# Kernel optimization log

Measured on AMD Instinct MI355X. Metric: run time of the kernel, lower is better.

## Reference

```python
import jax, jax.numpy as jnp
import numpy as np

T = 10
EPS = 1e-05

def setup_inputs() -> dict:
    key = jax.random.key(0)
    k1, k2 = jax.random.split(key)
    B, C, H, W = 128, 64, 56, 56
    X = jax.random.normal(k1, (B, C, H, W), dtype=jnp.float32)
    beta = jnp.zeros((C,), dtype=jnp.float32)
    return {"X": X, "beta": beta}


def reference(X, beta):
    # Training-path of BWItnBlock.forward (grad enabled branch of iter_norm_batch)
    B, C, H, W = X.shape
    d = C                      # n_channels, num_groups g = 1
    m = B * H * W
    # x = X.transpose(0,1).view(g, d, -1)  -> [d, m] with g=1
    x = jnp.transpose(X, (1, 0, 2, 3)).reshape(d, m)
    mean = jnp.mean(x, axis=1, keepdims=True)          # [d, 1]
    xc = x - mean                                      # [d, m]
    I = jnp.eye(d, dtype=X.dtype)
    # Sigma = eps*I + xc xc^T / m
    Sigma = EPS * I + (xc @ xc.T) / m                  # [d, d]
    # fix_cov: multiply off-diagonal by 0.9, diagonal by 1.0
    fix = 0.9 + 0.1 * I
    Sigma = Sigma * fix
    rTr = 1.0 / jnp.trace(Sigma)                       # scalar (sum(Sigma * I))
    Sigma_N = Sigma * rTr
    # Newton-Schulz iterations for inverse sqrt: P <- 1.5 P - 0.5 P^3 Sigma_N
    P = I
    for _ in range(T):
        P = 1.5 * P - 0.5 * ((P @ P @ P) @ Sigma_N)
    wm = P * jnp.sqrt(rTr)                             # whitening matrix [d, d]
    xn = wm @ xc                                       # [d, m]
    X_hat = jnp.transpose(xn.reshape(C, B, H, W), (1, 0, 2, 3))
    X_hat = X_hat + beta.reshape(1, C, 1, 1)
    return X_hat
```

## Files before the change

kernel.cpp:

```cpp
#include <hip/hip_runtime.h>

#define CH 64
#define HW 3136
#define MTOT 401408

typedef __attribute__((ext_vector_type(8))) short short8;
typedef __attribute__((ext_vector_type(4))) float f32x4;
typedef __attribute__((ext_vector_type(4))) unsigned int u32x4;

__device__ __forceinline__ void split8(const float4 a, const float4 b,
                                       short8& hi, short8& lo, float& ssum){
  const float f[8] = {a.x,a.y,a.z,a.w, b.x,b.y,b.z,b.w};
  u32x4 hp, lp;
#pragma unroll
  for (int j=0;j<4;++j){
    const unsigned int b0 = __float_as_uint(f[2*j]);
    const unsigned int b1 = __float_as_uint(f[2*j+1]);
    hp[j] = (b0 >> 16) | (b1 & 0xFFFF0000u);
    const float h0 = __uint_as_float(b0 & 0xFFFF0000u);
    const float h1 = __uint_as_float(b1 & 0xFFFF0000u);
    const unsigned int l0 = __float_as_uint(f[2*j]   - h0);
    const unsigned int l1 = __float_as_uint(f[2*j+1] - h1);
    lp[j] = (l0 >> 16) | (l1 & 0xFFFF0000u);
  }
  hi = __builtin_bit_cast(short8, hp);
  lo = __builtin_bit_cast(short8, lp);
  ssum += ((f[0]+f[1])+(f[2]+f[3])) + ((f[4]+f[5])+(f[6]+f[7]));
}

__global__ __launch_bounds__(256) void k1_cov(const float* __restrict__ X,
                                              float* __restrict__ SR){
  constexpr int RG[10] = {0,1,1,2,2,2,3,3,3,3};
  constexpr int CG[10] = {0,0,1,0,1,2,0,1,2,3};
  __shared__ float red[4096];
  __shared__ float chs[64];

  const int t   = threadIdx.x;
  const int wid = __builtin_amdgcn_readfirstlane(t >> 6);
  const int l   = t & 63;
  const int wg  = blockIdx.x * 4 + wid;
  const int lrow = l & 15;
  const int lk   = (l >> 4) * 8;

  f32x4 acc[10];
#pragma unroll
  for (int bi=0; bi<10; ++bi) acc[bi] = (f32x4){0.f,0.f,0.f,0.f};
  float sums[4] = {0.f,0.f,0.f,0.f};

  for (int i=0; i<4; ++i){
    const int s = wg*4 + i;
    const int b = s / 98;
    const int p = (s - b*98) * 32;
    const float* base = X + (size_t)b*(CH*HW) + p + lrow*HW + lk;
    short8 fh[4], fl[4];
#pragma unroll
    for (int g=0; g<4; ++g){
      const float* pg = base + (size_t)g*16*HW;
      const float4 v0 = *(const float4*)pg;
      const float4 v1 = *(const float4*)(pg + 4);
      split8(v0, v1, fh[g], fl[g], sums[g]);
    }
#pragma unroll
    for (int bi=0; bi<10; ++bi){
      acc[bi] = __builtin_amdgcn_mfma_f32_16x16x32_bf16(fh[RG[bi]], fh[CG[bi]], acc[bi], 0,0,0);
      acc[bi] = __builtin_amdgcn_mfma_f32_16x16x32_bf16(fh[RG[bi]], fl[CG[bi]], acc[bi], 0,0,0);
      acc[bi] = __builtin_amdgcn_mfma_f32_16x16x32_bf16(fl[RG[bi]], fh[CG[bi]], acc[bi], 0,0,0);
    }
  }

#pragma unroll
  for (int g=0; g<4; ++g){
    sums[g] += __shfl_xor(sums[g], 16);
    sums[g] += __shfl_xor(sums[g], 32);
  }

  for (int w=0; w<4; ++w){
    if (wid == w){
#pragma unroll
      for (int bi=0; bi<10; ++bi){
        const int row0 = RG[bi]*16 + 4*(l>>4);
        const int col  = CG[bi]*16 + (l&15);
#pragma unroll
        for (int r=0; r<4; ++r){
          float* d = &red[(row0+r)*64 + col];
          if (w==0) *d = acc[bi][r]; else *d += acc[bi][r];
        }
      }
      if (l < 16){
#pragma unroll
        for (int g=0; g<4; ++g){
          if (w==0) chs[g*16+l] = sums[g]; else chs[g*16+l] += sums[g];
        }
      }
    }
    __syncthreads();
  }

#pragma unroll
  for (int bi=0; bi<10; ++bi){
    const int r = RG[bi]*16 + (t>>4);
    const int c = CG[bi]*16 + (t&15);
    unsafeAtomicAdd(&SR[r*64+c], red[r*64+c]);
  }
  if (t < 64) unsafeAtomicAdd(&SR[4096+t], chs[t]);
}

__device__ __forceinline__ void mm_AtB(const float* a, const float* b, float* out,
                                       float alpha, const float* aff, float beta_){
  const int t = threadIdx.x;
  const int c2 = 2*(t & 31);
  const int r0 = 8*(t >> 5);
  float acc[8][2];
#pragma unroll
  for (int i=0;i<8;++i){ acc[i][0]=0.f; acc[i][1]=0.f; }
  for (int k=0;k<64;++k){
    const float2 bv = *(const float2*)&b[k*64 + c2];
    const float4 a0 = *(const float4*)&a[k*64 + r0];
    const float4 a1 = *(const float4*)&a[k*64 + r0 + 4];
    const float av[8] = {a0.x,a0.y,a0.z,a0.w, a1.x,a1.y,a1.z,a1.w};
#pragma unroll
    for (int i=0;i<8;++i){ acc[i][0] += av[i]*bv.x; acc[i][1] += av[i]*bv.y; }
  }
  float res[8][2];
#pragma unroll
  for (int i=0;i<8;++i){
    float f0 = alpha*acc[i][0], f1 = alpha*acc[i][1];
    if (aff){ f0 += beta_*aff[(r0+i)*64 + c2]; f1 += beta_*aff[(r0+i)*64 + c2 + 1]; }
    res[i][0]=f0; res[i][1]=f1;
  }
  __syncthreads();
#pragma unroll
  for (int i=0;i<8;++i){
    float2 o2; o2.x = res[i][0]; o2.y = res[i][1];
    *(float2*)&out[(r0+i)*64 + c2] = o2;
  }
  __syncthreads();
}

__global__ __launch_bounds__(256) void k2_wm(const float* __restrict__ SR,
                                             const float* __restrict__ beta,
                                             float* __restrict__ WMT,
                                             float* __restrict__ OFS){
  __shared__ __align__(16) float bufE[4096];
  __shared__ __align__(16) float bufA[4096];
  __shared__ __align__(16) float bufB[4096];
  __shared__ float meanv[64];
  __shared__ float scal[2];
  const int t = threadIdx.x;
  const float inv_m = 1.f/(float)MTOT;
  if (t < 64) meanv[t] = SR[4096 + t]*inv_m;
  __syncthreads();
  for (int idx=t; idx<4096; idx+=256){
    const int r = idx >> 6, c = idx & 63;
    const int src = ((r >> 4) >= (c >> 4)) ? idx : (c*64 + r);
    const float cov = SR[src]*inv_m - meanv[r]*meanv[c];
    bufE[idx] = (r==c) ? (cov + 1e-5f - 1.f) : 0.9f*cov;
  }
  __syncthreads();
  float n2 = 0.f, tr = 0.f;
  for (int idx=t; idx<4096; idx+=256){
    const float e = bufE[idx];
    n2 += e*e;
    if ((idx >> 6) == (idx & 63)) tr += e;
  }
  bufA[t] = n2; bufB[t] = tr;
  __syncthreads();
  if (t < 64){
    bufA[t] = bufA[t]+bufA[t+64]+bufA[t+128]+bufA[t+192];
    bufB[t] = bufB[t]+bufB[t+64]+bufB[t+128]+bufB[t+192];
  }
  __syncthreads();
  if (t == 0){
    float s1=0.f, s2=0.f;
    for (int i=0;i<64;++i){ s1 += bufA[i]; s2 += bufB[i]; }
    scal[0] = s1; scal[1] = s2;
  }
  __syncthreads();
  const float frob2 = scal[0];
  const float trE   = scal[1];
  float wscale = 1.f;
  const float* wmLds;
  if (frob2 < 0.04f){
    mm_AtB(bufE, bufE, bufA, 1.f, nullptr, 0.f);
    mm_AtB(bufA, bufE, bufB, 1.f, nullptr, 0.f);
    for (int idx=t; idx<4096; idx+=256){
      const int r = idx >> 6, c = idx & 63;
      bufB[idx] = ((r==c)?1.f:0.f) - 0.5f*bufE[idx] + 0.375f*bufA[idx] - 0.3125f*bufB[idx];
    }
    mm_AtB(bufA, bufA, bufE, 1.f, nullptr, 0.f);
    for (int idx=t; idx<4096; idx+=256)
      bufB[idx] += 0.2734375f*bufE[idx];
    wmLds = bufB;
  } else {
    const float rTr = 1.f/(trE + 64.f);
    for (int idx=t; idx<4096; idx+=256){
      const int r = idx >> 6, c = idx & 63;
      bufE[idx] = (bufE[idx] + ((r==c)?1.f:0.f))*rTr;
      bufA[idx] = (r==c)?1.f:0.f;
    }
    __syncthreads();
    for (int it=0; it<10; ++it){
      mm_AtB(bufA, bufE, bufB, 1.f, nullptr, 0.f);
      mm_AtB(bufA, bufB, bufB, 1.f, nullptr, 0.f);
      mm_AtB(bufA, bufB, bufA, -0.5f, bufA, 1.5f);
    }
    wscale = sqrtf(rTr);
    wmLds = bufA;
  }
  __syncthreads();
  for (int idx=t; idx<4096; idx+=256)
    WMT[(idx & 63)*64 + (idx >> 6)] = wmLds[idx]*wscale;
  if (t < 64){
    float d = 0.f;
    for (int j=0;j<64;++j) d += wmLds[t*64 + j]*meanv[j];
    OFS[t] = beta[t] - d*wscale;
  }
}

#define PXT 128
__global__ __launch_bounds__(256, 4) void k3_apply(const float* __restrict__ X,
                                                   const float* __restrict__ WMT,
                                                   const float* __restrict__ OFS,
                                                   float* __restrict__ out){
  __shared__ __align__(16) float tile[64*PXT];
  const int t = threadIdx.x;
  const int w = __builtin_amdgcn_readfirstlane((int)(t >> 6));
  const int l = t & 63;
  const int pxbase = blockIdx.x * PXT;

  {
    const int half = l >> 5;
    const int P    = pxbase + 4*(l & 31);
    const int b    = P / HW;
    const int hw   = P - b*HW;
    const float* src0 = X + (size_t)b*(CH*HW) + hw;
#pragma unroll
    for (int j=0;j<8;++j){
      const int cr = 16*w + 2*j;
      __builtin_amdgcn_global_load_lds(
        (const __attribute__((address_space(1))) unsigned int*)(src0 + (size_t)(cr + half)*HW),
        (__attribute__((address_space(3))) unsigned int*)&tile[cr*PXT],
        16, 0, 0);
    }
  }
  asm volatile("s_waitcnt vmcnt(0)" ::: "memory");
  __syncthreads();

  const int c0 = 16*w;
  float acc[16][2];
#pragma unroll
  for (int i=0;i<16;++i){ acc[i][0]=0.f; acc[i][1]=0.f; }
  for (int k=0;k<64;++k){
    const float2 xv = *(const float2*)&tile[k*PXT + 2*l];
    const float* wr = &WMT[k*64 + c0];
#pragma unroll
    for (int i=0;i<16;++i){
      acc[i][0] += wr[i]*xv.x;
      acc[i][1] += wr[i]*xv.y;
    }
  }

  const int P2  = pxbase + 2*l;
  const int b2  = P2 / HW;
  const int hw2 = P2 - b2*HW;
  float* ob = out + (size_t)b2*(CH*HW) + hw2;
#pragma unroll
  for (int i=0;i<16;++i){
    const float o = OFS[c0+i];
    float2 pk; pk.x = acc[i][0]+o; pk.y = acc[i][1]+o;
    *(float2*)(ob + (size_t)(c0+i)*HW) = pk;
  }
}

extern "C" void kernel_launch(void* const* d_in, const int* in_sizes, int n_in,
                              void* d_out, int out_size, void* d_ws, size_t ws_size,
                              hipStream_t stream){
  const float* X    = (const float*)d_in[0];
  const float* beta = (const float*)d_in[1];
  float* out = (float*)d_out;
  float* ws  = (float*)d_ws;
  float* SR  = ws;
  float* WMT = ws + 4160;
  float* OFS = WMT + 4096;
  hipMemsetAsync(SR, 0, 4160*sizeof(float), stream);
  hipLaunchKernelGGL(k1_cov,   dim3(784),  dim3(256), 0, stream, X, SR);
  hipLaunchKernelGGL(k2_wm,    dim3(1),    dim3(256), 0, stream, SR, beta, WMT, OFS);
  hipLaunchKernelGGL(k3_apply, dim3(3136), dim3(256), 0, stream, X, WMT, OFS, out);
}
```

Measured before the change: 250.5 us.

## Double-buffer LDS staging with persistent blocks in covariance and apply kernels

Both the covariance kernel and the apply kernel now use 392 persistent blocks, each looping over 8 pixel tiles. The next tile is prefetched into a second LDS buffer with global_load_lds while the current one is computed. In the covariance kernel, X was previously read straight from global memory into registers; it now goes through a swizzled LDS layout meant to avoid bank conflicts. The goal is to hide memory latency and cut per-block launch overhead, at the cost of double the LDS per block (lower occupancy) and fewer blocks to spread across CUs.

```diff
diff --git a/kernel.cpp b/kernel.cpp
--- a/kernel.cpp
+++ b/kernel.cpp
@@ -3,6 +3,9 @@
 #define CH 64
 #define HW 3136
 #define MTOT 401408
+#define TPX 128
+#define NBLK 392
+#define TPB 8
 
 typedef __attribute__((ext_vector_type(8))) short short8;
 typedef __attribute__((ext_vector_type(4))) float f32x4;
@@ -32,32 +35,53 @@
                                               float* __restrict__ SR){
   constexpr int RG[10] = {0,1,1,2,2,2,3,3,3,3};
   constexpr int CG[10] = {0,0,1,0,1,2,0,1,2,3};
-  __shared__ float red[4096];
+  __shared__ __align__(16) float buf[2][64*TPX];
   __shared__ float chs[64];
 
   const int t   = threadIdx.x;
   const int wid = __builtin_amdgcn_readfirstlane(t >> 6);
   const int l   = t & 63;
-  const int wg  = blockIdx.x * 4 + wid;
-  const int lrow = l & 15;
-  const int lk   = (l >> 4) * 8;
+  const int lr  = l & 15;
+  const int q   = l >> 4;
 
   f32x4 acc[10];
 #pragma unroll
   for (int bi=0; bi<10; ++bi) acc[bi] = (f32x4){0.f,0.f,0.f,0.f};
   float sums[4] = {0.f,0.f,0.f,0.f};
 
-  for (int i=0; i<4; ++i){
-    const int s = wg*4 + i;
-    const int b = s / 98;
-    const int p = (s - b*98) * 32;
-    const float* base = X + (size_t)b*(CH*HW) + p + lrow*HW + lk;
+  auto stage = [&](int tl, float* dst){
+    const unsigned mbase = (unsigned)(blockIdx.x*TPB + tl) * TPX;
+#pragma unroll
+    for (int j=0;j<8;++j){
+      const int r  = 16*wid + 2*j + (l>>5);
+      const int cb = (l&31) ^ (r&7);
+      const unsigned m  = mbase + 4*cb;
+      const unsigned b  = m / HW;
+      const unsigned hw = m - b*HW;
+      const float* src = X + (size_t)b*(CH*HW) + (size_t)r*HW + hw;
+      __builtin_amdgcn_global_load_lds(
+        (const __attribute__((address_space(1))) unsigned int*)src,
+        (__attribute__((address_space(3))) unsigned int*)(dst + (16*wid + 2*j)*TPX),
+        16, 0, 0);
+    }
+  };
+
+  stage(0, buf[0]);
+  asm volatile("s_waitcnt vmcnt(0)" ::: "memory");
+  __syncthreads();
+
+  int pb = 0;
+  for (int tl=0; tl<TPB; ++tl){
+    if (tl+1 < TPB) stage(tl+1, buf[pb^1]);
+    const char* bp = (const char*)buf[pb];
     short8 fh[4], fl[4];
 #pragma unroll
     for (int g=0; g<4; ++g){
-      const float* pg = base + (size_t)g*16*HW;
-      const float4 v0 = *(const float4*)pg;
-      const float4 v1 = *(const float4*)(pg + 4);
+      const int r   = 16*g + lr;
+      const int sw  = r & 7;
+      const int cb0 = 8*wid + 2*q;
+      const float4 v0 = *(const float4*)(bp + r*512 + 16*((cb0+0)^sw));
+      const float4 v1 = *(const float4*)(bp + r*512 + 16*((cb0+1)^sw));
       split8(v0, v1, fh[g], fl[g], sums[g]);
     }
 #pragma unroll
@@ -66,6 +90,9 @@
       acc[bi] = __builtin_amdgcn_mfma_f32_16x16x32_bf16(fh[RG[bi]], fl[CG[bi]], acc[bi], 0,0,0);
       acc[bi] = __builtin_amdgcn_mfma_f32_16x16x32_bf16(fl[RG[bi]], fh[CG[bi]], acc[bi], 0,0,0);
     }
+    asm volatile("s_waitcnt vmcnt(0)" ::: "memory");
+    __syncthreads();
+    pb ^= 1;
   }
 
 #pragma unroll
@@ -74,12 +101,13 @@
     sums[g] += __shfl_xor(sums[g], 32);
   }
 
+  float* red = &buf[0][0];
   for (int w=0; w<4; ++w){
     if (wid == w){
 #pragma unroll
       for (int bi=0; bi<10; ++bi){
-        const int row0 = RG[bi]*16 + 4*(l>>4);
-        const int col  = CG[bi]*16 + (l&15);
+        const int row0 = RG[bi]*16 + 4*q;
+        const int col  = CG[bi]*16 + lr;
 #pragma unroll
         for (int r=0; r<4; ++r){
           float* d = &red[(row0+r)*64 + col];
@@ -217,58 +245,70 @@
   }
 }
 
-#define PXT 128
-__global__ __launch_bounds__(256, 4) void k3_apply(const float* __restrict__ X,
-                                                   const float* __restrict__ WMT,
-                                                   const float* __restrict__ OFS,
-                                                   float* __restrict__ out){
-  __shared__ __align__(16) float tile[64*PXT];
+__global__ __launch_bounds__(256) void k3_apply(const float* __restrict__ X,
+                                                const float* __restrict__ WMT,
+                                                const float* __restrict__ OFS,
+                                                float* __restrict__ out){
+  __shared__ __align__(16) float buf[2][64*TPX];
   const int t = threadIdx.x;
   const int w = __builtin_amdgcn_readfirstlane((int)(t >> 6));
   const int l = t & 63;
-  const int pxbase = blockIdx.x * PXT;
-
-  {
-    const int half = l >> 5;
-    const int P    = pxbase + 4*(l & 31);
-    const int b    = P / HW;
-    const int hw   = P - b*HW;
-    const float* src0 = X + (size_t)b*(CH*HW) + hw;
+  const int c0 = 16*w;
+
+  float ofs[16];
+#pragma unroll
+  for (int i=0;i<16;++i) ofs[i] = OFS[c0+i];
+
+  auto stage = [&](int tl, float* dst){
+    const unsigned mbase = (unsigned)(blockIdx.x*TPB + tl) * TPX;
 #pragma unroll
     for (int j=0;j<8;++j){
-      const int cr = 16*w + 2*j;
+      const int r  = 16*w + 2*j + (l>>5);
+      const unsigned m  = mbase + 4*(l&31);
+      const unsigned b  = m / HW;
+      const unsigned hw = m - b*HW;
+      const float* src = X + (size_t)b*(CH*HW) + (size_t)r*HW + hw;
       __builtin_amdgcn_global_load_lds(
-        (const __attribute__((address_space(1))) unsigned int*)(src0 + (size_t)(cr + half)*HW),
-        (__attribute__((address_space(3))) unsigned int*)&tile[cr*PXT],
+        (const __attribute__((address_space(1))) unsigned int*)src,
+        (__attribute__((address_space(3))) unsigned int*)(dst + (16*w + 2*j)*TPX),
         16, 0, 0);
     }
-  }
+  };
+
+  stage(0, buf[0]);
   asm volatile("s_waitcnt vmcnt(0)" ::: "memory");
   __syncthreads();
 
-  const int c0 = 16*w;
-  float acc[16][2];
-#pragma unroll
-  for (int i=0;i<16;++i){ acc[i][0]=0.f; acc[i][1]=0.f; }
-  for (int k=0;k<64;++k){
-    const float2 xv = *(const float2*)&tile[k*PXT + 2*l];
-    const float* wr = &WMT[k*64 + c0];
-#pragma unroll
-    for (int i=0;i<16;++i){
-      acc[i][0] += wr[i]*xv.x;
-      acc[i][1] += wr[i]*xv.y;
-    }
-  }
-
-  const int P2  = pxbase + 2*l;
-  const int b2  = P2 / HW;
-  const int hw2 = P2 - b2*HW;
-  float* ob = out + (size_t)b2*(CH*HW) + hw2;
-#pragma unroll
-  for (int i=0;i<16;++i){
-    const float o = OFS[c0+i];
-    float2 pk; pk.x = acc[i][0]+o; pk.y = acc[i][1]+o;
-    *(float2*)(ob + (size_t)(c0+i)*HW) = pk;
+  int pb = 0;
+  for (int tl=0; tl<TPB; ++tl){
+    if (tl+1 < TPB) stage(tl+1, buf[pb^1]);
+    const float* bp = buf[pb];
+    float acc[16][2];
+#pragma unroll
+    for (int i=0;i<16;++i){ acc[i][0]=0.f; acc[i][1]=0.f; }
+    for (int k=0;k<64;++k){
+      const float2 xv = *(const float2*)&bp[k*TPX + 2*l];
+      const float* wr = &WMT[k*64 + c0];
+#pragma unroll
+      for (int i=0;i<16;++i){
+        acc[i][0] += wr[i]*xv.x;
+        acc[i][1] += wr[i]*xv.y;
+      }
+    }
+    {
+      const unsigned P2 = (unsigned)(blockIdx.x*TPB + tl)*TPX + 2*l;
+      const unsigned b2 = P2 / HW;
+      const unsigned hw2 = P2 - b2*HW;
+      float* ob = out + (size_t)b2*(CH*HW) + hw2;
+#pragma unroll
+      for (int i=0;i<16;++i){
+        float2 pk; pk.x = acc[i][0]+ofs[i]; pk.y = acc[i][1]+ofs[i];
+        *(float2*)(ob + (size_t)(c0+i)*HW) = pk;
+      }
+    }
+    asm volatile("s_waitcnt vmcnt(0)" ::: "memory");
+    __syncthreads();
+    pb ^= 1;
   }
 }
 
@@ -283,7 +323,7 @@
   float* WMT = ws + 4160;
   float* OFS = WMT + 4096;
   hipMemsetAsync(SR, 0, 4160*sizeof(float), stream);
-  hipLaunchKernelGGL(k1_cov,   dim3(784),  dim3(256), 0, stream, X, SR);
+  hipLaunchKernelGGL(k1_cov,   dim3(NBLK), dim3(256), 0, stream, X, SR);
   hipLaunchKernelGGL(k2_wm,    dim3(1),    dim3(256), 0, stream, SR, beta, WMT, OFS);
-  hipLaunchKernelGGL(k3_apply, dim3(3136), dim3(256), 0, stream, X, WMT, OFS, out);
-}
+  hipLaunchKernelGGL(k3_apply, dim3(NBLK), dim3(256), 0, stream, X, WMT, OFS, out);
+}
```

Result: slower. 260.1 us (+3.8%).
